# Kernel tuning notes

Measured on AMD Instinct MI355X. Metric: run time of the kernel, lower is better.

## Reference

```python
import jax, jax.numpy as jnp
import numpy as np

DIM = 1024
N_HEADS = 16
B, T = 2, 2048


def setup_inputs() -> dict:
    key = jax.random.key(0)
    ks = jax.random.split(key, 9)
    D, H = DIM, N_HEADS
    return {
        "x": jax.random.normal(ks[0], (B, T, D), dtype=jnp.float32),
        "W_in": jax.random.normal(ks[1], (3 * D + H, D), dtype=jnp.float32) * (1.0 / np.sqrt(D)),
        "conv_w": jax.random.normal(ks[2], (D, 1, 4), dtype=jnp.float32) * 0.5,  # depthwise, groups=D
        "conv_b": jax.random.normal(ks[3], (D,), dtype=jnp.float32) * 0.1,
        "decay_param": jax.random.normal(ks[4], (H,), dtype=jnp.float32) * 0.5 - 3.0,
        "gn_w": jnp.ones((D,), dtype=jnp.float32),
        "gn_b": jnp.zeros((D,), dtype=jnp.float32),
        "W_out": jax.random.normal(ks[5], (D, D), dtype=jnp.float32) * (1.0 / np.sqrt(D)),
    }


def reference(x, W_in, conv_w, conv_b, decay_param, gn_w, gn_b, W_out):
    Bs, Ts, D = x.shape
    H = decay_param.shape[0]
    K = D // H
    scale = 1.0 / np.sqrt(D)

    proj = x @ W_in.T                                   # (B,T,3D+H)
    r, v, k, w = jnp.split(proj, [D, 2 * D, 3 * D], axis=-1)

    # depthwise causal-ish conv: F.pad(3 left) + Conv1d(padding=3) => left pad 6, take first T
    k_in = jnp.transpose(k, (0, 2, 1))                  # (B,D,T)
    k_out = jax.lax.conv_general_dilated(
        k_in, conv_w, window_strides=(1,), padding=[(6, 0)],
        dimension_numbers=("NCH", "OIH", "NCH"), feature_group_count=D)
    k_out = k_out[:, :, :Ts] + conv_b[None, :, None]
    k_out = jnp.transpose(k_out, (0, 2, 1))             # (B,T,D)

    v = v * jax.nn.silu(k_out)

    decay_gate = jax.nn.sigmoid(decay_param[None, None, :] + w)  # (B,T,H)
    log_decay = -8.0 * (1.0 - decay_gate) - 0.1
    ld = jnp.transpose(log_decay, (0, 2, 1))            # (B,H,T)

    v_in = jnp.transpose(v.reshape(Bs, Ts, H, K), (0, 2, 1, 3)) * scale  # (B,H,T,K)

    # parallel scan via causal decay matrix
    cs = jnp.cumsum(ld, axis=-1)                        # (B,H,T)
    idx = jnp.arange(Ts)
    mask = idx[:, None] >= idx[None, :]                 # (T,T) causal
    L = cs[..., :, None] - cs[..., None, :]             # (B,H,T,T)
    Wd = jnp.where(mask, jnp.exp(jnp.where(mask, L, 0.0)), 0.0)
    y = jnp.einsum("bhts,bhsk->bhtk", Wd, v_in)         # (B,H,T,K)

    y = jnp.transpose(y, (0, 2, 1, 3)).reshape(Bs, Ts, D)
    out = jax.nn.silu(r) * y                            # (B,T,D)

    # GroupNorm(H groups) over channels, applied on (B,D,T)
    o = jnp.transpose(out, (0, 2, 1)).reshape(Bs, H, K, Ts)
    mean = jnp.mean(o, axis=(2, 3), keepdims=True)
    var = jnp.var(o, axis=(2, 3), keepdims=True)
    o = (o - mean) * jax.lax.rsqrt(var + 1e-5)
    o = o * gn_w.reshape(1, H, K, 1) + gn_b.reshape(1, H, K, 1)
    out = jnp.transpose(o.reshape(Bs, D, Ts), (0, 2, 1))

    return out @ W_out.T
```

## Files before the change

kernel.cpp:

```cpp
#include <hip/hip_runtime.h>

#define D_   1024
#define H_   16
#define T_   2048
#define B_   2
#define BT_  (B_*T_)
#define NIN_ 3088
#define NP_  3200
#define CHUNK_ 64
#define NCH_  (T_/CHUNK_)
#define GN_INV (1.0f/131072.0f)
#define NBLK_C 4096

typedef unsigned short u16;
typedef __attribute__((ext_vector_type(8))) __bf16 bf16x8;
typedef __attribute__((ext_vector_type(8))) unsigned short u16x8;
typedef __attribute__((ext_vector_type(4))) unsigned short u16x4;
typedef __attribute__((ext_vector_type(4))) float  f32x4;

struct __align__(16) F4 { float x, y, z, w; };
struct __align__(8)  U4 { u16 x, y, z, w; };

__device__ inline u16 f2bf(float f) {
  union { float f; unsigned u; } q; q.f = f;
  unsigned r = q.u + 0x7FFFu + ((q.u >> 16) & 1u);
  return (u16)(r >> 16);
}
__device__ inline float bf2f(u16 v) {
  union { unsigned u; float f; } q; q.u = ((unsigned)v) << 16; return q.f;
}

__device__ inline void gl_lds16(const void* g, void* l) {
  __builtin_amdgcn_global_load_lds(
      (const __attribute__((address_space(1))) unsigned*)g,
      (__attribute__((address_space(3))) unsigned*)l, 16, 0, 0);
}

__global__ void cvt_all(const float* __restrict__ x, const float* __restrict__ W_in,
                        const float* __restrict__ W_out,
                        u16* __restrict__ xb, u16* __restrict__ wb, u16* __restrict__ wob) {
  const int nx = BT_ * D_ / 4, nw = NP_ * D_ / 4, no = D_ * D_ / 4;
  int q = blockIdx.x * 256 + threadIdx.x;
  if (q < nx) {
    int i = q * 4;
    F4 f = *reinterpret_cast<const F4*>(x + i);
    U4 u; u.x = f2bf(f.x); u.y = f2bf(f.y); u.z = f2bf(f.z); u.w = f2bf(f.w);
    *reinterpret_cast<U4*>(xb + i) = u;
  } else if (q < nx + nw) {
    int i = (q - nx) * 4;
    int row = i >> 10;
    U4 u; u.x = 0; u.y = 0; u.z = 0; u.w = 0;
    if (row < NIN_) {
      F4 f = *reinterpret_cast<const F4*>(W_in + i);
      u.x = f2bf(f.x); u.y = f2bf(f.y); u.z = f2bf(f.z); u.w = f2bf(f.w);
    }
    *reinterpret_cast<U4*>(wb + i) = u;
  } else if (q < nx + nw + no) {
    int i = (q - nx - nw) * 4;
    F4 f = *reinterpret_cast<const F4*>(W_out + i);
    U4 u; u.x = f2bf(f.x); u.y = f2bf(f.y); u.z = f2bf(f.z); u.w = f2bf(f.w);
    *reinterpret_cast<U4*>(wob + i) = u;
  }
}

template<bool BF16OUT>
__global__ __launch_bounds__(256, 2) void gemm_bt(
    const u16* __restrict__ A, const u16* __restrict__ Bm,
    void* __restrict__ Cv, int M, int N, int K) {
  __shared__ __align__(16) u16 As[128 * 64];
  __shared__ __align__(16) u16 Bs[128 * 64];
  const int tid  = threadIdx.x;
  const int lane = tid & 63;
  const int wid  = tid >> 6;
  const int tm = blockIdx.y * 128, tn = blockIdx.x * 128;
  const int wm = (wid >> 1) * 64,  wn = (wid & 1) * 64;
  const int krow = lane & 15;
  const int ksub = (lane >> 4) * 8;
  f32x4 acc[4][4] = {};

  for (int kt = 0; kt < K; kt += 64) {
#pragma unroll
    for (int i = 0; i < 4; ++i) {
      int e = i * 2048 + tid * 8;
      int r = e >> 6;
      int c = (((tid & 7) ^ (r & 7)) << 3);
      gl_lds16(A  + (size_t)(tm + r) * K + kt + c, &As[e]);
      gl_lds16(Bm + (size_t)(tn + r) * K + kt + c, &Bs[e]);
    }
    __syncthreads();
#pragma unroll
    for (int kk = 0; kk < 64; kk += 32) {
      bf16x8 af[4], bfr[4];
#pragma unroll
      for (int i = 0; i < 4; ++i) {
        int row = wm + i * 16 + krow;
        int b = (((kk + ksub) >> 3) ^ (row & 7)) << 3;
        af[i] = *reinterpret_cast<const bf16x8*>(&As[row * 64 + b]);
      }
#pragma unroll
      for (int i = 0; i < 4; ++i) {
        int row = wn + i * 16 + krow;
        int b = (((kk + ksub) >> 3) ^ (row & 7)) << 3;
        bfr[i] = *reinterpret_cast<const bf16x8*>(&Bs[row * 64 + b]);
      }
#pragma unroll
      for (int mi = 0; mi < 4; ++mi)
#pragma unroll
        for (int ni = 0; ni < 4; ++ni)
          acc[mi][ni] = __builtin_amdgcn_mfma_f32_16x16x32_bf16(af[mi], bfr[ni], acc[mi][ni], 0, 0, 0);
    }
    __syncthreads();
  }
  const int rb = tm + wm + (lane >> 4) * 4;
  const int cb = tn + wn + (lane & 15);
#pragma unroll
  for (int mi = 0; mi < 4; ++mi)
#pragma unroll
    for (int ni = 0; ni < 4; ++ni)
#pragma unroll
      for (int j = 0; j < 4; ++j) {
        size_t off = (size_t)(rb + mi * 16 + j) * N + cb + ni * 16;
        if constexpr (BF16OUT) ((u16*)Cv)[off] = f2bf(acc[mi][ni][j]);
        else                   ((float*)Cv)[off] = acc[mi][ni][j];
      }
}

__global__ void scanA_kernel(const u16* __restrict__ proj,
                             const float* __restrict__ conv_w,
                             const float* __restrict__ conv_b,
                             const float* __restrict__ decay,
                             u16* __restrict__ vv,
                             float* __restrict__ ye, float* __restrict__ Pc,
                             float* __restrict__ pfx) {
  __shared__ __align__(16) u16 lv[CHUNK_ * 64];
  __shared__ __align__(16) u16 lk[(CHUNK_ + 8) * 64];
  int bh = blockIdx.x >> 5, c = blockIdx.x & 31;
  int b = bh >> 4, h = bh & 15;
  int k = threadIdx.x;
  int d0 = h * 64;
  int t0 = c * CHUNK_;
  int rsub = k >> 3, cblk = (k & 7) * 8;
#pragma unroll
  for (int it = 0; it < 8; ++it) {
    int r = it * 8 + rsub;
    *reinterpret_cast<u16x8*>(&lv[r * 64 + cblk]) =
      *reinterpret_cast<const u16x8*>(&proj[(size_t)(b * T_ + t0 + r) * NP_ + 1024 + d0 + cblk]);
  }
#pragma unroll
  for (int it = 0; it < 9; ++it) {
    int r = it * 8 + rsub;
    int tt = t0 + r - 6;
    u16x8 kv = {0, 0, 0, 0, 0, 0, 0, 0};
    if (tt >= 0 && tt < T_)
      kv = *reinterpret_cast<const u16x8*>(&proj[(size_t)(b * T_ + tt) * NP_ + 2048 + d0 + cblk]);
    *reinterpret_cast<u16x8*>(&lk[r * 64 + cblk]) = kv;
  }
  float wv = bf2f(proj[(size_t)(b * T_ + t0 + k) * NP_ + 3072 + h]);
  float gte = 1.f / (1.f + __expf(-(decay[h] + wv)));
  float my_a = __expf(-8.f * (1.f - gte) - 0.1f);
  int d = d0 + k;
  float cw0 = conv_w[d * 4], cw1 = conv_w[d * 4 + 1],
        cw2 = conv_w[d * 4 + 2], cw3 = conv_w[d * 4 + 3];
  float cb = conv_b[d];
  __syncthreads();
  u16* V = vv + ((size_t)bh * T_ + t0) * 64 + k;
  float k0 = bf2f(lk[0 * 64 + k]), k1 = bf2f(lk[1 * 64 + k]), k2 = bf2f(lk[2 * 64 + k]);
  float y = 0.f, pf = 1.f, my_pf = 1.f;
#pragma unroll
  for (int i = 0; i < CHUNK_; ++i) {
    float k3 = bf2f(lk[(i + 3) * 64 + k]);
    float v  = bf2f(lv[i * 64 + k]);
    float kc = cb;
    kc = fmaf(k0, cw0, kc); kc = fmaf(k1, cw1, kc);
    kc = fmaf(k2, cw2, kc); kc = fmaf(k3, cw3, kc);
    float sil = kc / (1.f + __expf(-kc));
    float g = v * sil * (1.f / 32.f);
    float a = __shfl(my_a, i);
    y = fmaf(a, y, g);
    V[(size_t)i * 64] = f2bf(y);
    pf *= a;
    if (i == k) my_pf = pf;
    k0 = k1; k1 = k2; k2 = k3;
  }
  pfx[(size_t)bh * T_ + t0 + k] = my_pf;
  ye[(size_t)blockIdx.x * 64 + k] = y;
  Pc[(size_t)blockIdx.x * 64 + k] = pf;
}

__global__ void comb_kernel(const float* __restrict__ ye, const float* __restrict__ Pc,
                            float* __restrict__ cin) {
  int g4 = blockIdx.x * 256 + threadIdx.x;
  int bh = g4 >> 4, k4 = (g4 & 15) * 4;
  f32x4 s = {0.f, 0.f, 0.f, 0.f};
  for (int c = 0; c < NCH_; ++c) {
    size_t i = ((size_t)bh * NCH_ + c) * 64 + k4;
    *reinterpret_cast<f32x4*>(&cin[i]) = s;
    f32x4 e = *reinterpret_cast<const f32x4*>(&ye[i]);
    f32x4 p = *reinterpret_cast<const f32x4*>(&Pc[i]);
    s = e + p * s;
  }
}

__global__ void applyC_kernel(const u16* __restrict__ vv, const u16* __restrict__ proj,
                              const float* __restrict__ pfx, const float* __restrict__ cin,
                              u16* __restrict__ ob, float* __restrict__ part) {
  int idx4 = blockIdx.x * 256 + threadIdx.x;
  int k4 = (idx4 & 15) * 4;
  int t  = (idx4 >> 4) & 2047;
  int bh = idx4 >> 15;
  int b = bh >> 4, h = bh & 15;
  size_t ebase = ((size_t)bh * T_ + t) * 64 + k4;
  f32x4 ci = *reinterpret_cast<const f32x4*>(&cin[(((size_t)bh * NCH_) + (t >> 6)) * 64 + k4]);
  float px = pfx[(size_t)bh * T_ + t];
  u16x4 yv = *reinterpret_cast<const u16x4*>(&vv[ebase]);
  u16x4 rv = *reinterpret_cast<const u16x4*>(&proj[(size_t)(b * T_ + t) * NP_ + h * 64 + k4]);
  u16x4 ov;
  float s1 = 0.f, s2 = 0.f;
#pragma unroll
  for (int j = 0; j < 4; ++j) {
    float yf = fmaf(px, ci[j], bf2f(yv[j]));
    float r = bf2f(rv[j]);
    float o = yf * (r / (1.f + __expf(-r)));
    ov[j] = f2bf(o);
    s1 += o; s2 += o * o;
  }
  *reinterpret_cast<u16x4*>(&ob[ebase]) = ov;
#pragma unroll
  for (int m = 32; m; m >>= 1) { s1 += __shfl_xor(s1, m); s2 += __shfl_xor(s2, m); }
  __shared__ float ps[8];
  int wid = threadIdx.x >> 6, lane = threadIdx.x & 63;
  if (lane == 0) { ps[wid] = s1; ps[4 + wid] = s2; }
  __syncthreads();
  if (threadIdx.x == 0) {
    part[blockIdx.x]          = ps[0] + ps[1] + ps[2] + ps[3];
    part[NBLK_C + blockIdx.x] = ps[4] + ps[5] + ps[6] + ps[7];
  }
}

__global__ void reduce_kernel(const float* __restrict__ part, float* __restrict__ sums) {
  int bh = blockIdx.x;
  int t = threadIdx.x;
  int base = bh * 128;
  float s1 = part[base + t]           + part[base + 64 + t];
  float s2 = part[NBLK_C + base + t]  + part[NBLK_C + base + 64 + t];
#pragma unroll
  for (int m = 32; m; m >>= 1) { s1 += __shfl_xor(s1, m); s2 += __shfl_xor(s2, m); }
  if (t == 0) { sums[bh] = s1; sums[32 + bh] = s2; }
}

__global__ void applyD_kernel(const u16* __restrict__ ob, const float* __restrict__ sums,
                              const float* __restrict__ gn_w, const float* __restrict__ gn_b,
                              u16* __restrict__ on) {
  int idx4 = blockIdx.x * 256 + threadIdx.x;
  int k4 = (idx4 & 15) * 4;
  int t  = (idx4 >> 4) & 2047;
  int bh = idx4 >> 15;
  int b = bh >> 4, h = bh & 15;
  float mean = sums[bh] * GN_INV;
  float var  = sums[32 + bh] * GN_INV - mean * mean;
  float inv  = rsqrtf(var + 1e-5f);
  int d = h * 64 + k4;
  u16x4 o = *reinterpret_cast<const u16x4*>(&ob[((size_t)bh * T_ + t) * 64 + k4]);
  F4 gw = *reinterpret_cast<const F4*>(&gn_w[d]);
  F4 gb = *reinterpret_cast<const F4*>(&gn_b[d]);
  u16x4 r;
  r[0] = f2bf((bf2f(o[0]) - mean) * inv * gw.x + gb.x);
  r[1] = f2bf((bf2f(o[1]) - mean) * inv * gw.y + gb.y);
  r[2] = f2bf((bf2f(o[2]) - mean) * inv * gw.z + gb.z);
  r[3] = f2bf((bf2f(o[3]) - mean) * inv * gw.w + gb.w);
  *reinterpret_cast<u16x4*>(&on[(size_t)(b * T_ + t) * D_ + d]) = r;
}

extern "C" void kernel_launch(void* const* d_in, const int* in_sizes, int n_in,
                              void* d_out, int out_size, void* d_ws, size_t ws_size,
                              hipStream_t stream) {
  const float* x      = (const float*)d_in[0];
  const float* W_in   = (const float*)d_in[1];
  const float* conv_w = (const float*)d_in[2];
  const float* conv_b = (const float*)d_in[3];
  const float* decay  = (const float*)d_in[4];
  const float* gn_w   = (const float*)d_in[5];
  const float* gn_b   = (const float*)d_in[6];
  const float* W_out  = (const float*)d_in[7];

  char* p = (char*)d_ws;
  auto alloc = [&](size_t bytes) { void* r = (void*)p; p += (bytes + 255) & ~(size_t)255; return r; };
  u16*  xb   = (u16*)alloc((size_t)BT_ * D_ * 2);
  u16*  wb   = (u16*)alloc((size_t)NP_ * D_ * 2);
  u16*  wob  = (u16*)alloc((size_t)D_ * D_ * 2);
  u16*  proj = (u16*)alloc((size_t)BT_ * NP_ * 2);
  u16*  vv   = (u16*)alloc((size_t)BT_ * D_ * 2);
  u16*  ob   = (u16*)alloc((size_t)BT_ * D_ * 2);
  float* pfx  = (float*)alloc((size_t)B_ * H_ * T_ * 4);
  float* ye   = (float*)alloc((size_t)B_ * H_ * NCH_ * 64 * 4);
  float* Pc   = (float*)alloc((size_t)B_ * H_ * NCH_ * 64 * 4);
  float* cin  = (float*)alloc((size_t)B_ * H_ * NCH_ * 64 * 4);
  float* part = (float*)alloc((size_t)2 * NBLK_C * 4);
  float* sums = (float*)alloc(64 * 4);
  u16*  on   = xb;

  if ((size_t)(p - (char*)d_ws) > ws_size) return;

  const int nq = (BT_ * D_ + NP_ * D_ + D_ * D_) / 4;
  hipLaunchKernelGGL(cvt_all, dim3((nq + 255) / 256), dim3(256), 0, stream,
                     x, W_in, W_out, xb, wb, wob);
  hipLaunchKernelGGL((gemm_bt<true>),  dim3(NP_ / 128, BT_ / 128), dim3(256), 0, stream,
                     xb, wb, (void*)proj, BT_, NP_, D_);
  hipLaunchKernelGGL(scanA_kernel,  dim3(B_ * H_ * NCH_), dim3(64),  0, stream,
                     proj, conv_w, conv_b, decay, vv, ye, Pc, pfx);
  hipLaunchKernelGGL(comb_kernel,   dim3(2),              dim3(256), 0, stream, ye, Pc, cin);
  hipLaunchKernelGGL(applyC_kernel, dim3(NBLK_C),         dim3(256), 0, stream, vv, proj, pfx, cin, ob, part);
  hipLaunchKernelGGL(reduce_kernel, dim3(32),             dim3(64),  0, stream, part, sums);
  hipLaunchKernelGGL(applyD_kernel, dim3(BT_ * D_ / 1024), dim3(256), 0, stream, ob, sums, gn_w, gn_b, on);
  hipLaunchKernelGGL((gemm_bt<false>), dim3(D_ / 128, BT_ / 128), dim3(256), 0, stream,
                     on, wob, d_out, BT_, D_, D_);
}
```

Before: 176.0 us.

## Swizzle GEMM tile order, narrow output GEMM tile, widen elementwise vectors, spread comb

The GEMM now uses a 1D grid whose block index is remapped so that consecutive blocks are spread across the 8 XCDs. It also takes a template N-tile width, and the output projection uses 64-wide tiles so it launches more blocks. The elementwise applyC/applyD kernels now process 8 bf16 values per thread with 16-byte accesses, which halves the block count and the partial-sum count. comb_kernel now runs as 32 blocks with one thread per channel instead of 2 blocks of float4 threads, giving more parallel lanes for the serial chunk scan.

```diff
diff --git a/kernel.cpp b/kernel.cpp
--- a/kernel.cpp
+++ b/kernel.cpp
@@ -10,7 +10,7 @@
 #define CHUNK_ 64
 #define NCH_  (T_/CHUNK_)
 #define GN_INV (1.0f/131072.0f)
-#define NBLK_C 4096
+#define NBLK_C 2048
 
 typedef unsigned short u16;
 typedef __attribute__((ext_vector_type(8))) __bf16 bf16x8;
@@ -63,20 +63,24 @@
   }
 }
 
-template<bool BF16OUT>
+template<bool BF16OUT, int TN>
 __global__ __launch_bounds__(256, 2) void gemm_bt(
     const u16* __restrict__ A, const u16* __restrict__ Bm,
     void* __restrict__ Cv, int M, int N, int K) {
+  constexpr int NI = TN / 32;
   __shared__ __align__(16) u16 As[128 * 64];
-  __shared__ __align__(16) u16 Bs[128 * 64];
+  __shared__ __align__(16) u16 Bs[TN * 64];
   const int tid  = threadIdx.x;
   const int lane = tid & 63;
   const int wid  = tid >> 6;
-  const int tm = blockIdx.y * 128, tn = blockIdx.x * 128;
-  const int wm = (wid >> 1) * 64,  wn = (wid & 1) * 64;
+  const int nwg = gridDim.x;
+  const int s = (blockIdx.x & 7) * (nwg >> 3) + (blockIdx.x >> 3);
+  const int MT = M >> 7;
+  const int tm = (s % MT) * 128, tn = (s / MT) * TN;
+  const int wm = (wid >> 1) * 64,  wn = (wid & 1) * (TN / 2);
   const int krow = lane & 15;
   const int ksub = (lane >> 4) * 8;
-  f32x4 acc[4][4] = {};
+  f32x4 acc[4][NI] = {};
 
   for (int kt = 0; kt < K; kt += 64) {
 #pragma unroll
@@ -84,13 +88,19 @@
       int e = i * 2048 + tid * 8;
       int r = e >> 6;
       int c = (((tid & 7) ^ (r & 7)) << 3);
-      gl_lds16(A  + (size_t)(tm + r) * K + kt + c, &As[e]);
+      gl_lds16(A + (size_t)(tm + r) * K + kt + c, &As[e]);
+    }
+#pragma unroll
+    for (int i = 0; i < NI; ++i) {
+      int e = i * 2048 + tid * 8;
+      int r = e >> 6;
+      int c = (((tid & 7) ^ (r & 7)) << 3);
       gl_lds16(Bm + (size_t)(tn + r) * K + kt + c, &Bs[e]);
     }
     __syncthreads();
 #pragma unroll
     for (int kk = 0; kk < 64; kk += 32) {
-      bf16x8 af[4], bfr[4];
+      bf16x8 af[4], bfr[NI];
 #pragma unroll
       for (int i = 0; i < 4; ++i) {
         int row = wm + i * 16 + krow;
@@ -98,7 +108,7 @@
         af[i] = *reinterpret_cast<const bf16x8*>(&As[row * 64 + b]);
       }
 #pragma unroll
-      for (int i = 0; i < 4; ++i) {
+      for (int i = 0; i < NI; ++i) {
         int row = wn + i * 16 + krow;
         int b = (((kk + ksub) >> 3) ^ (row & 7)) << 3;
         bfr[i] = *reinterpret_cast<const bf16x8*>(&Bs[row * 64 + b]);
@@ -106,7 +116,7 @@
 #pragma unroll
       for (int mi = 0; mi < 4; ++mi)
 #pragma unroll
-        for (int ni = 0; ni < 4; ++ni)
+        for (int ni = 0; ni < NI; ++ni)
           acc[mi][ni] = __builtin_amdgcn_mfma_f32_16x16x32_bf16(af[mi], bfr[ni], acc[mi][ni], 0, 0, 0);
     }
     __syncthreads();
@@ -116,7 +126,7 @@
 #pragma unroll
   for (int mi = 0; mi < 4; ++mi)
 #pragma unroll
-    for (int ni = 0; ni < 4; ++ni)
+    for (int ni = 0; ni < NI; ++ni)
 #pragma unroll
       for (int j = 0; j < 4; ++j) {
         size_t off = (size_t)(rb + mi * 16 + j) * N + cb + ni * 16;
@@ -189,42 +199,44 @@
 
 __global__ void comb_kernel(const float* __restrict__ ye, const float* __restrict__ Pc,
                             float* __restrict__ cin) {
-  int g4 = blockIdx.x * 256 + threadIdx.x;
-  int bh = g4 >> 4, k4 = (g4 & 15) * 4;
-  f32x4 s = {0.f, 0.f, 0.f, 0.f};
+  int bh = blockIdx.x;
+  int k = threadIdx.x;
+  float s = 0.f;
+#pragma unroll 8
   for (int c = 0; c < NCH_; ++c) {
-    size_t i = ((size_t)bh * NCH_ + c) * 64 + k4;
-    *reinterpret_cast<f32x4*>(&cin[i]) = s;
-    f32x4 e = *reinterpret_cast<const f32x4*>(&ye[i]);
-    f32x4 p = *reinterpret_cast<const f32x4*>(&Pc[i]);
-    s = e + p * s;
+    size_t i = ((size_t)bh * NCH_ + c) * 64 + k;
+    cin[i] = s;
+    s = ye[i] + Pc[i] * s;
   }
 }
 
 __global__ void applyC_kernel(const u16* __restrict__ vv, const u16* __restrict__ proj,
                               const float* __restrict__ pfx, const float* __restrict__ cin,
                               u16* __restrict__ ob, float* __restrict__ part) {
-  int idx4 = blockIdx.x * 256 + threadIdx.x;
-  int k4 = (idx4 & 15) * 4;
-  int t  = (idx4 >> 4) & 2047;
-  int bh = idx4 >> 15;
+  int idx8 = blockIdx.x * 256 + threadIdx.x;
+  int k8 = (idx8 & 7) * 8;
+  int t  = (idx8 >> 3) & 2047;
+  int bh = idx8 >> 14;
   int b = bh >> 4, h = bh & 15;
-  size_t ebase = ((size_t)bh * T_ + t) * 64 + k4;
-  f32x4 ci = *reinterpret_cast<const f32x4*>(&cin[(((size_t)bh * NCH_) + (t >> 6)) * 64 + k4]);
+  size_t ebase = ((size_t)bh * T_ + t) * 64 + k8;
+  size_t cibase = (((size_t)bh * NCH_) + (t >> 6)) * 64 + k8;
+  f32x4 ciA = *reinterpret_cast<const f32x4*>(&cin[cibase]);
+  f32x4 ciB = *reinterpret_cast<const f32x4*>(&cin[cibase + 4]);
   float px = pfx[(size_t)bh * T_ + t];
-  u16x4 yv = *reinterpret_cast<const u16x4*>(&vv[ebase]);
-  u16x4 rv = *reinterpret_cast<const u16x4*>(&proj[(size_t)(b * T_ + t) * NP_ + h * 64 + k4]);
-  u16x4 ov;
+  u16x8 yv = *reinterpret_cast<const u16x8*>(&vv[ebase]);
+  u16x8 rv = *reinterpret_cast<const u16x8*>(&proj[(size_t)(b * T_ + t) * NP_ + h * 64 + k8]);
+  u16x8 ov;
   float s1 = 0.f, s2 = 0.f;
 #pragma unroll
-  for (int j = 0; j < 4; ++j) {
-    float yf = fmaf(px, ci[j], bf2f(yv[j]));
+  for (int j = 0; j < 8; ++j) {
+    float ci = (j < 4) ? ciA[j] : ciB[j - 4];
+    float yf = fmaf(px, ci, bf2f(yv[j]));
     float r = bf2f(rv[j]);
     float o = yf * (r / (1.f + __expf(-r)));
     ov[j] = f2bf(o);
     s1 += o; s2 += o * o;
   }
-  *reinterpret_cast<u16x4*>(&ob[ebase]) = ov;
+  *reinterpret_cast<u16x8*>(&ob[ebase]) = ov;
 #pragma unroll
   for (int m = 32; m; m >>= 1) { s1 += __shfl_xor(s1, m); s2 += __shfl_xor(s2, m); }
   __shared__ float ps[8];
@@ -240,9 +252,9 @@
 __global__ void reduce_kernel(const float* __restrict__ part, float* __restrict__ sums) {
   int bh = blockIdx.x;
   int t = threadIdx.x;
-  int base = bh * 128;
-  float s1 = part[base + t]           + part[base + 64 + t];
-  float s2 = part[NBLK_C + base + t]  + part[NBLK_C + base + 64 + t];
+  int base = bh * 64;
+  float s1 = part[base + t];
+  float s2 = part[NBLK_C + base + t];
 #pragma unroll
   for (int m = 32; m; m >>= 1) { s1 += __shfl_xor(s1, m); s2 += __shfl_xor(s2, m); }
   if (t == 0) { sums[bh] = s1; sums[32 + bh] = s2; }
@@ -251,24 +263,28 @@
 __global__ void applyD_kernel(const u16* __restrict__ ob, const float* __restrict__ sums,
                               const float* __restrict__ gn_w, const float* __restrict__ gn_b,
                               u16* __restrict__ on) {
-  int idx4 = blockIdx.x * 256 + threadIdx.x;
-  int k4 = (idx4 & 15) * 4;
-  int t  = (idx4 >> 4) & 2047;
-  int bh = idx4 >> 15;
+  int idx8 = blockIdx.x * 256 + threadIdx.x;
+  int k8 = (idx8 & 7) * 8;
+  int t  = (idx8 >> 3) & 2047;
+  int bh = idx8 >> 14;
   int b = bh >> 4, h = bh & 15;
   float mean = sums[bh] * GN_INV;
   float var  = sums[32 + bh] * GN_INV - mean * mean;
   float inv  = rsqrtf(var + 1e-5f);
-  int d = h * 64 + k4;
-  u16x4 o = *reinterpret_cast<const u16x4*>(&ob[((size_t)bh * T_ + t) * 64 + k4]);
-  F4 gw = *reinterpret_cast<const F4*>(&gn_w[d]);
-  F4 gb = *reinterpret_cast<const F4*>(&gn_b[d]);
-  u16x4 r;
-  r[0] = f2bf((bf2f(o[0]) - mean) * inv * gw.x + gb.x);
-  r[1] = f2bf((bf2f(o[1]) - mean) * inv * gw.y + gb.y);
-  r[2] = f2bf((bf2f(o[2]) - mean) * inv * gw.z + gb.z);
-  r[3] = f2bf((bf2f(o[3]) - mean) * inv * gw.w + gb.w);
-  *reinterpret_cast<u16x4*>(&on[(size_t)(b * T_ + t) * D_ + d]) = r;
+  int d = h * 64 + k8;
+  u16x8 o = *reinterpret_cast<const u16x8*>(&ob[((size_t)bh * T_ + t) * 64 + k8]);
+  f32x4 gwA = *reinterpret_cast<const f32x4*>(&gn_w[d]);
+  f32x4 gwB = *reinterpret_cast<const f32x4*>(&gn_w[d + 4]);
+  f32x4 gbA = *reinterpret_cast<const f32x4*>(&gn_b[d]);
+  f32x4 gbB = *reinterpret_cast<const f32x4*>(&gn_b[d + 4]);
+  u16x8 r;
+#pragma unroll
+  for (int j = 0; j < 8; ++j) {
+    float gw = (j < 4) ? gwA[j] : gwB[j - 4];
+    float gb = (j < 4) ? gbA[j] : gbB[j - 4];
+    r[j] = f2bf((bf2f(o[j]) - mean) * inv * gw + gb);
+  }
+  *reinterpret_cast<u16x8*>(&on[(size_t)(b * T_ + t) * D_ + d]) = r;
 }
 
 extern "C" void kernel_launch(void* const* d_in, const int* in_sizes, int n_in,
@@ -304,14 +320,14 @@
   const int nq = (BT_ * D_ + NP_ * D_ + D_ * D_) / 4;
   hipLaunchKernelGGL(cvt_all, dim3((nq + 255) / 256), dim3(256), 0, stream,
                      x, W_in, W_out, xb, wb, wob);
-  hipLaunchKernelGGL((gemm_bt<true>),  dim3(NP_ / 128, BT_ / 128), dim3(256), 0, stream,
+  hipLaunchKernelGGL((gemm_bt<true, 128>), dim3((NP_ / 128) * (BT_ / 128)), dim3(256), 0, stream,
                      xb, wb, (void*)proj, BT_, NP_, D_);
   hipLaunchKernelGGL(scanA_kernel,  dim3(B_ * H_ * NCH_), dim3(64),  0, stream,
                      proj, conv_w, conv_b, decay, vv, ye, Pc, pfx);
-  hipLaunchKernelGGL(comb_kernel,   dim3(2),              dim3(256), 0, stream, ye, Pc, cin);
+  hipLaunchKernelGGL(comb_kernel,   dim3(32),             dim3(64),  0, stream, ye, Pc, cin);
   hipLaunchKernelGGL(applyC_kernel, dim3(NBLK_C),         dim3(256), 0, stream, vv, proj, pfx, cin, ob, part);
   hipLaunchKernelGGL(reduce_kernel, dim3(32),             dim3(64),  0, stream, part, sums);
-  hipLaunchKernelGGL(applyD_kernel, dim3(BT_ * D_ / 1024), dim3(256), 0, stream, ob, sums, gn_w, gn_b, on);
-  hipLaunchKernelGGL((gemm_bt<false>), dim3(D_ / 128, BT_ / 128), dim3(256), 0, stream,
+  hipLaunchKernelGGL(applyD_kernel, dim3(BT_ * D_ / 2048), dim3(256), 0, stream, ob, sums, gn_w, gn_b, on);
+  hipLaunchKernelGGL((gemm_bt<false, 64>), dim3((D_ / 64) * (BT_ / 128)), dim3(256), 0, stream,
                      on, wob, d_out, BT_, D_, D_);
 }
```

Result: faster. 171.6 us (-2.5%).
